# Optimization experiments

Measured on AMD Instinct MI355X. Metric: run time of the kernel, lower is better.

## Reference

```python
import jax, jax.numpy as jnp
import numpy as np

H = 128      # hidden_dim
N = 200000   # number of available (job, machine) ops
M = 1000     # machine nodes
J = 5000     # job nodes


def setup_inputs() -> dict:
    key = jax.random.key(0)
    ks = jax.random.split(key, 8)
    s = 0.05  # weight scale
    return {
        "x_graph": jax.random.normal(ks[0], (1, 2 * H), jnp.float32),
        "x_m": jax.random.normal(ks[1], (M, H), jnp.float32),
        "x_job": jax.random.normal(ks[2], (J, H), jnp.float32),
        "m_ids": jax.random.randint(ks[3], (N,), 0, M),
        "job_idx": jax.random.randint(ks[4], (N,), 0, J),
        "W0": jax.random.normal(ks[5], (4 * H, H), jnp.float32) * s,
        "b0": jnp.zeros((H,), jnp.float32),
        "W1": jax.random.normal(ks[6], (H, H), jnp.float32) * s,
        "b1": jnp.zeros((H,), jnp.float32),
        "W2": jax.random.normal(ks[7], (H, 1), jnp.float32) * s,
        "b2": jnp.zeros((1,), jnp.float32),
    }


def reference(x_graph, x_m, x_job, m_ids, job_idx, W0, b0, W1, b1, W2, b2):
    n = m_ids.shape[0]
    # vectorized form of the python loop: [x_graph | x_m[m_id] | x_job[job_pos]] -> [N, 4H]
    feats = jnp.concatenate(
        [
            jnp.broadcast_to(x_graph, (n, x_graph.shape[1])),
            x_m[m_ids],
            x_job[job_idx],
        ],
        axis=1,
    )
    h = jax.nn.relu(feats @ W0 + b0)   # Linear(4H -> H) + ReLU
    h = jax.nn.relu(h @ W1 + b1)       # Linear(H -> H) + ReLU
    scores = (h @ W2 + b2)[:, 0]       # Linear(H -> 1), squeeze -> [N]
    logp = jax.nn.log_softmax(scores, axis=0)
    probs = jnp.exp(logp)
    idx = jnp.argmax(scores)           # greedy selection (deterministic baseline)
    entropy = -jnp.sum(probs * logp)   # Categorical entropy
    return idx, probs[idx], logp[idx], entropy
```

## Files before the change

kernel.cpp:

```cpp
#include <hip/hip_runtime.h>
#include <math.h>

#define HID 128
#define TILE_R 64
#define TILE_P 32
#define XS_STRIDE 132
#define H0S_STRIDE 136
#define DELTA 0.05f
#define MAIN_GRID 1024

typedef short bf16x8 __attribute__((ext_vector_type(8)));
typedef float f32x4 __attribute__((ext_vector_type(4)));

static __device__ __forceinline__ unsigned short f2bf(float f) {
    union { float f; unsigned u; } v; v.f = f;
    unsigned r = v.u + 0x7FFFu + ((v.u >> 16) & 1u);
    return (unsigned short)(r >> 16);
}
static __device__ __forceinline__ float bflo(unsigned u) {
    union { unsigned u; float f; } v; v.u = u << 16; return v.f;
}
static __device__ __forceinline__ float bfhi(unsigned u) {
    union { unsigned u; float f; } v; v.u = u & 0xFFFF0000u; return v.f;
}

#define FMA4(avc, wv)                         \
    acc[r][0] = fmaf(avc, wv.x, acc[r][0]);   \
    acc[r][1] = fmaf(avc, wv.y, acc[r][1]);   \
    acc[r][2] = fmaf(avc, wv.z, acc[r][2]);   \
    acc[r][3] = fmaf(avc, wv.w, acc[r][3]);

__global__ __launch_bounds__(256, 4) void precompute_kernel(
    const float* __restrict__ x_graph,
    const float* __restrict__ x_m,
    const float* __restrict__ x_job,
    const float* __restrict__ W0,
    const float* __restrict__ b0,
    const float* __restrict__ W1,
    float* __restrict__ g,
    unsigned short* __restrict__ Pbf,
    unsigned short* __restrict__ W1T,
    int M, int J, int aTiles, int bTiles)
{
    const int t = threadIdx.x;
    const int bid = blockIdx.x;

    if (bid == 0) {
        __shared__ float xg[2 * HID];
        if (t < HID) { xg[t] = x_graph[t]; xg[t + HID] = x_graph[t + HID]; }
        __syncthreads();
        if (t < HID) {
            float acc = b0[t];
            #pragma unroll 8
            for (int k = 0; k < 2 * HID; ++k)
                acc = fmaf(xg[k], W0[k * HID + t], acc);
            g[t] = acc;
        }
        return;
    }
    if (bid == 1 + aTiles + bTiles) {
        for (int e = t; e < HID * HID; e += 256) {
            int n = e >> 7, k = e & 127;
            W1T[e] = f2bf(W1[k * HID + n]);
        }
        return;
    }

    const int tb = bid - 1;
    const float* X;
    const float* W;
    int r0, nr, dstBase;
    if (tb < aTiles) {
        r0 = tb * TILE_P;
        nr = min(TILE_P, M - r0);
        X = x_m + (size_t)r0 * HID;
        W = W0 + 2 * HID * HID;
        dstBase = r0;
    } else {
        int jb = tb - aTiles;
        r0 = jb * TILE_P;
        nr = min(TILE_P, J - r0);
        X = x_job + (size_t)r0 * HID;
        W = W0 + 3 * HID * HID;
        dstBase = M + r0;
    }

    __shared__ float xs[TILE_P * XS_STRIDE];
    {
        int row = t >> 3;
        int e = t & 7;
        #pragma unroll
        for (int u = 0; u < 4; ++u) {
            int c = e * 16 + u * 4;
            float4 v = (row < nr) ? *(const float4*)(X + row * HID + c)
                                  : make_float4(0.f, 0.f, 0.f, 0.f);
            *(float4*)&xs[row * XS_STRIDE + c] = v;
        }
    }
    __syncthreads();

    const int w = t >> 6;
    const int l = t & 63;
    const int tc = l & 7;
    const int tr = l >> 3;
    const int c0 = w * 32 + tc * 4;

    float acc[4][4];
    #pragma unroll
    for (int r = 0; r < 4; ++r)
        #pragma unroll
        for (int c = 0; c < 4; ++c) acc[r][c] = 0.0f;

    #pragma unroll 2
    for (int k0 = 0; k0 < HID; k0 += 4) {
        float4 w0v = *(const float4*)(W + (k0 + 0) * HID + c0);
        float4 w1v = *(const float4*)(W + (k0 + 1) * HID + c0);
        float4 w2m = *(const float4*)(W + (k0 + 2) * HID + c0);
        float4 w3v = *(const float4*)(W + (k0 + 3) * HID + c0);
        #pragma unroll
        for (int r = 0; r < 4; ++r) {
            float4 a = *(const float4*)&xs[(r * 8 + tr) * XS_STRIDE + k0];
            FMA4(a.x, w0v)
            FMA4(a.y, w1v)
            FMA4(a.z, w2m)
            FMA4(a.w, w3v)
        }
    }

    #pragma unroll
    for (int r = 0; r < 4; ++r) {
        int row = r * 8 + tr;
        if (row < nr) {
            unsigned lo0 = (unsigned)f2bf(acc[r][0]) | ((unsigned)f2bf(acc[r][1]) << 16);
            unsigned lo1 = (unsigned)f2bf(acc[r][2]) | ((unsigned)f2bf(acc[r][3]) << 16);
            uint2 pk = make_uint2(lo0, lo1);
            *(uint2*)(Pbf + (size_t)(dstBase + row) * HID + c0) = pk;
        }
    }
}

__global__ __launch_bounds__(256, 4) void main_kernel(
    const int* __restrict__ m_ids,
    const int* __restrict__ job_idx,
    const float* __restrict__ b1,
    const float* __restrict__ W2,
    const float* __restrict__ b2,
    const float* __restrict__ g,
    const unsigned short* __restrict__ Pbf,
    const unsigned short* __restrict__ W1T,
    float* __restrict__ scores,
    float4* __restrict__ partials,
    float* __restrict__ tmax,
    int N, int M, int tiles)
{
    __shared__ __align__(16) short h0s[TILE_R * H0S_STRIDE];
    __shared__ float sred[4 * TILE_R];

    const int t = threadIdx.x;
    const int l = t & 63;
    const int w = t >> 6;
    const int quad = l >> 4;
    const int mrow = l & 15;

    bf16x8 bfr[2][4];
    {
        const unsigned short* wb = W1T + (size_t)(w * 32 + mrow) * HID + quad * 8;
        #pragma unroll
        for (int nt = 0; nt < 2; ++nt)
            #pragma unroll
            for (int kc = 0; kc < 4; ++kc)
                bfr[nt][kc] = *(const bf16x8*)(wb + nt * 16 * HID + kc * 32);
    }
    const float b1v0 = b1[w * 32 + mrow];
    const float b1v1 = b1[w * 32 + 16 + mrow];
    const float w2v0 = W2[w * 32 + mrow];
    const float w2v1 = W2[w * 32 + 16 + mrow];
    const float b2v = b2[0];

    for (int tile = blockIdx.x; tile < tiles; tile += MAIN_GRID) {
        const int row0 = tile * TILE_R;

        {
            int row = t >> 2;
            int q = t & 3;
            int grow = row0 + row;
            int gr = (grow < N) ? grow : (N - 1);
            int m = m_ids[gr];
            int j = job_idx[gr];
            const unsigned short* pm = Pbf + (size_t)m * HID + q * 32;
            const unsigned short* pj = Pbf + (size_t)(M + j) * HID + q * 32;
            const float* gp = g + q * 32;
            short* dst = &h0s[row * H0S_STRIDE + q * 32];
            #pragma unroll
            for (int u = 0; u < 4; ++u) {
                uint4 mv = *(const uint4*)(pm + u * 8);
                uint4 jv = *(const uint4*)(pj + u * 8);
                float4 g0 = *(const float4*)(gp + u * 8);
                float4 g1 = *(const float4*)(gp + u * 8 + 4);
                float h0v = fmaxf(bflo(mv.x) + bflo(jv.x) + g0.x, 0.f);
                float h1v = fmaxf(bfhi(mv.x) + bfhi(jv.x) + g0.y, 0.f);
                float h2v = fmaxf(bflo(mv.y) + bflo(jv.y) + g0.z, 0.f);
                float h3v = fmaxf(bfhi(mv.y) + bfhi(jv.y) + g0.w, 0.f);
                float h4v = fmaxf(bflo(mv.z) + bflo(jv.z) + g1.x, 0.f);
                float h5v = fmaxf(bfhi(mv.z) + bfhi(jv.z) + g1.y, 0.f);
                float h6v = fmaxf(bflo(mv.w) + bflo(jv.w) + g1.z, 0.f);
                float h7v = fmaxf(bfhi(mv.w) + bfhi(jv.w) + g1.w, 0.f);
                uint4 pk;
                pk.x = (unsigned)f2bf(h0v) | ((unsigned)f2bf(h1v) << 16);
                pk.y = (unsigned)f2bf(h2v) | ((unsigned)f2bf(h3v) << 16);
                pk.z = (unsigned)f2bf(h4v) | ((unsigned)f2bf(h5v) << 16);
                pk.w = (unsigned)f2bf(h6v) | ((unsigned)f2bf(h7v) << 16);
                *(uint4*)(dst + u * 8) = pk;
            }
        }
        __syncthreads();

        f32x4 acc[4][2];
        #pragma unroll
        for (int mt = 0; mt < 4; ++mt) {
            f32x4 z = {0.f, 0.f, 0.f, 0.f};
            acc[mt][0] = z;
            acc[mt][1] = z;
        }
        #pragma unroll
        for (int mt = 0; mt < 4; ++mt) {
            const short* ab = &h0s[(mt * 16 + mrow) * H0S_STRIDE + quad * 8];
            #pragma unroll
            for (int kc = 0; kc < 4; ++kc) {
                bf16x8 af = *(const bf16x8*)(ab + kc * 32);
                acc[mt][0] = __builtin_amdgcn_mfma_f32_16x16x32_bf16(af, bfr[0][kc], acc[mt][0], 0, 0, 0);
                acc[mt][1] = __builtin_amdgcn_mfma_f32_16x16x32_bf16(af, bfr[1][kc], acc[mt][1], 0, 0, 0);
            }
        }

        #pragma unroll
        for (int mt = 0; mt < 4; ++mt) {
            float p[4];
            #pragma unroll
            for (int i = 0; i < 4; ++i) {
                p[i] = fmaxf(acc[mt][0][i] + b1v0, 0.f) * w2v0
                     + fmaxf(acc[mt][1][i] + b1v1, 0.f) * w2v1;
            }
            #pragma unroll
            for (int off = 1; off < 16; off <<= 1) {
                #pragma unroll
                for (int i = 0; i < 4; ++i)
                    p[i] += __shfl_xor(p[i], off);
            }
            if (mrow == 0) {
                int rb = mt * 16 + quad * 4;
                sred[w * TILE_R + rb + 0] = p[0];
                sred[w * TILE_R + rb + 1] = p[1];
                sred[w * TILE_R + rb + 2] = p[2];
                sred[w * TILE_R + rb + 3] = p[3];
            }
        }
        __syncthreads();

        if (t < 64) {
            int grow = row0 + t;
            float s = sred[t] + sred[64 + t] + sred[128 + t] + sred[192 + t] + b2v;
            if (grow < N) scores[grow] = s;
            else s = -1e30f;

            float mmax = s;
            int midx = grow;
            #pragma unroll
            for (int off = 1; off < 64; off <<= 1) {
                float om = __shfl_xor(mmax, off);
                int oi = __shfl_xor(midx, off);
                if (om > mmax || (om == mmax && oi < midx)) { mmax = om; midx = oi; }
            }
            float d = s - mmax;
            float e = expf(d);
            float z = e;
            float ss = d * e;
            #pragma unroll
            for (int off = 1; off < 64; off <<= 1) {
                z += __shfl_xor(z, off);
                ss += __shfl_xor(ss, off);
            }
            if (t == 0) {
                partials[tile] = make_float4(mmax, z, ss, (float)midx);
                tmax[tile] = mmax;
            }
        }
    }
}

__device__ inline void sm_merge(float& am, float& az, float& ass, int& ai,
                                float bm, float bz, float bss, int bi)
{
    if (bm > am || (bm == am && bi < ai)) {
        float tm = am, tz = az, ts = ass; int ti = ai;
        am = bm; az = bz; ass = bss; ai = bi;
        bm = tm; bz = tz; bss = ts; bi = ti;
    }
    float f = expf(bm - am);
    az += bz * f;
    ass += (bss + (bm - am) * bz) * f;
}

__global__ __launch_bounds__(256) void scan_kernel(
    const float* __restrict__ tmax, int nparts,
    const float* __restrict__ scores,
    const int* __restrict__ m_ids,
    const int* __restrict__ job_idx,
    const float* __restrict__ x_m,
    const float* __restrict__ x_job,
    const float* __restrict__ W0,
    const float* __restrict__ W1,
    const float* __restrict__ b1,
    const float* __restrict__ W2,
    const float* __restrict__ b2,
    const float* __restrict__ g,
    float2* __restrict__ bests,
    int N)
{
    __shared__ int cand[256];
    __shared__ int ccount;
    __shared__ float rs[4];
    __shared__ int ri[4];
    __shared__ float mmx[4];

    const int t = threadIdx.x;
    const int w = t >> 6;
    const int l = t & 63;
    const int base = blockIdx.x * 256;

    float m0 = -1e30f, m1 = -1e30f, m2 = -1e30f, m3 = -1e30f;
    int i = t;
    for (; i + 768 < nparts; i += 1024) {
        m0 = fmaxf(m0, tmax[i]);
        m1 = fmaxf(m1, tmax[i + 256]);
        m2 = fmaxf(m2, tmax[i + 512]);
        m3 = fmaxf(m3, tmax[i + 768]);
    }
    for (; i < nparts; i += 256) m0 = fmaxf(m0, tmax[i]);
    float mhat = fmaxf(fmaxf(m0, m1), fmaxf(m2, m3));
    #pragma unroll
    for (int off = 1; off < 64; off <<= 1)
        mhat = fmaxf(mhat, __shfl_xor(mhat, off));
    if (l == 0) mmx[w] = mhat;
    if (t == 0) ccount = 0;
    __syncthreads();
    mhat = fmaxf(fmaxf(mmx[0], mmx[1]), fmaxf(mmx[2], mmx[3]));
    const float cut = mhat - DELTA;

    int idx = base + t;
    if (idx < N && scores[idx] >= cut) {
        int p = atomicAdd(&ccount, 1);
        cand[p] = idx;
    }
    __syncthreads();
    const int nc = ccount;
    if (nc == 0) {
        if (t == 0) bests[blockIdx.x] = make_float2(-1e30f, __int_as_float(0x7fffffff));
        return;
    }

    float bs = -1e30f;
    int bi = 0x7fffffff;
    for (int c = w; c < nc; c += 4) {
        int gr = cand[c];
        int mm = m_ids[gr];
        int jj = job_idx[gr];
        const float* xm = x_m + (size_t)mm * HID;
        const float* xj = x_job + (size_t)jj * HID;
        const float* wm = W0 + 2 * HID * HID;
        const float* wj = W0 + 3 * HID * HID;
        float a0 = g[l], a1 = g[l + 64];
        for (int k = 0; k < HID; ++k) {
            float xmk = xm[k];
            float xjk = xj[k];
            a0 = fmaf(xmk, wm[k * HID + l], a0);
            a1 = fmaf(xmk, wm[k * HID + l + 64], a1);
            a0 = fmaf(xjk, wj[k * HID + l], a0);
            a1 = fmaf(xjk, wj[k * HID + l + 64], a1);
        }
        a0 = fmaxf(a0, 0.f);
        a1 = fmaxf(a1, 0.f);
        float acc0 = 0.f, acc1 = 0.f;
        for (int k = 0; k < 64; ++k) {
            float h = __shfl(a0, k);
            acc0 = fmaf(h, W1[k * HID + l], acc0);
            acc1 = fmaf(h, W1[k * HID + l + 64], acc1);
        }
        for (int k = 0; k < 64; ++k) {
            float h = __shfl(a1, k);
            acc0 = fmaf(h, W1[(k + 64) * HID + l], acc0);
            acc1 = fmaf(h, W1[(k + 64) * HID + l + 64], acc1);
        }
        float p = fmaxf(acc0 + b1[l], 0.f) * W2[l]
                + fmaxf(acc1 + b1[l + 64], 0.f) * W2[l + 64];
        #pragma unroll
        for (int off = 1; off < 64; off <<= 1)
            p += __shfl_xor(p, off);
        float s = p + b2[0];
        if (s > bs || (s == bs && gr < bi)) { bs = s; bi = gr; }
    }
    if (l == 0) { rs[w] = bs; ri[w] = bi; }
    __syncthreads();
    if (t == 0) {
        float best = rs[0];
        int bwin = ri[0];
        for (int i2 = 1; i2 < 4; ++i2)
            if (rs[i2] > best || (rs[i2] == best && ri[i2] < bwin)) {
                best = rs[i2]; bwin = ri[i2];
            }
        bests[blockIdx.x] = make_float2(best, __int_as_float(bwin));
    }
}

__global__ __launch_bounds__(256) void finalize_kernel(
    const float4* __restrict__ partials, int nparts,
    const float2* __restrict__ bests, int nblocks,
    float* __restrict__ out)
{
    __shared__ float4 wred[4];
    __shared__ int widx[4];
    __shared__ float rs[4];
    __shared__ int ri[4];
    const int t = threadIdx.x;
    const int w = t >> 6;
    const int l = t & 63;

    float m = -1e30f, z = 0.f, ss = 0.f;
    int idx = 0x7fffffff;
    for (int i = t; i < nparts; i += 256) {
        float4 p = partials[i];
        sm_merge(m, z, ss, idx, p.x, p.y, p.z, (int)p.w);
    }
    #pragma unroll
    for (int off = 1; off < 64; off <<= 1) {
        float om = __shfl_xor(m, off);
        float oz = __shfl_xor(z, off);
        float os = __shfl_xor(ss, off);
        int oi = __shfl_xor(idx, off);
        sm_merge(m, z, ss, idx, om, oz, os, oi);
    }
    if (l == 0) { wred[w] = make_float4(m, z, ss, 0.f); widx[w] = idx; }

    float bs = -1e30f;
    int bi = 0x7fffffff;
    for (int i = t; i < nblocks; i += 256) {
        float2 b = bests[i];
        int gi = __float_as_int(b.y);
        if (b.x > bs || (b.x == bs && gi < bi)) { bs = b.x; bi = gi; }
    }
    #pragma unroll
    for (int off = 1; off < 64; off <<= 1) {
        float os = __shfl_xor(bs, off);
        int oi = __shfl_xor(bi, off);
        if (os > bs || (os == bs && oi < bi)) { bs = os; bi = oi; }
    }
    if (l == 0) { rs[w] = bs; ri[w] = bi; }
    __syncthreads();

    if (t == 0) {
        for (int i = 1; i < 4; ++i) {
            sm_merge(m, z, ss, idx, wred[i].x, wred[i].y, wred[i].z, widx[i]);
            if (rs[i] > bs || (rs[i] == bs && ri[i] < bi)) { bs = rs[i]; bi = ri[i]; }
        }
        float logZ = logf(z);
        out[0] = (float)bi;
        out[1] = expf(bs - m) / z;
        out[2] = (bs - m) - logZ;
        out[3] = logZ - ss / z;
    }
}

extern "C" void kernel_launch(void* const* d_in, const int* in_sizes, int n_in,
                              void* d_out, int out_size, void* d_ws, size_t ws_size,
                              hipStream_t stream)
{
    const float* x_graph = (const float*)d_in[0];
    const float* x_m     = (const float*)d_in[1];
    const float* x_job   = (const float*)d_in[2];
    const int*   m_ids   = (const int*)d_in[3];
    const int*   job_idx = (const int*)d_in[4];
    const float* W0      = (const float*)d_in[5];
    const float* b0      = (const float*)d_in[6];
    const float* W1      = (const float*)d_in[7];
    const float* b1      = (const float*)d_in[8];
    const float* W2      = (const float*)d_in[9];
    const float* b2      = (const float*)d_in[10];
    float* out = (float*)d_out;

    const int N = in_sizes[3];
    const int M = in_sizes[1] / HID;
    const int J = in_sizes[2] / HID;

    const int tiles = (N + TILE_R - 1) / TILE_R;
    const int aTiles = (M + TILE_P - 1) / TILE_P;
    const int bTiles = (J + TILE_P - 1) / TILE_P;
    const int sblocks = (N + 255) / 256;

    float* ws = (float*)d_ws;
    float* g = ws;
    float* scores = ws + HID;
    float4* partials = (float4*)(scores + N);
    float* tmax = (float*)(partials + tiles);
    const int tmaxPad = (tiles + 3) & ~3;
    float2* bests = (float2*)(tmax + tmaxPad);
    unsigned short* W1T = (unsigned short*)(bests + sblocks + (sblocks & 1));
    unsigned short* Pbf = W1T + HID * HID;

    precompute_kernel<<<1 + aTiles + bTiles + 1, 256, 0, stream>>>(
        x_graph, x_m, x_job, W0, b0, W1, g, Pbf, W1T, M, J, aTiles, bTiles);
    main_kernel<<<MAIN_GRID, 256, 0, stream>>>(
        m_ids, job_idx, b1, W2, b2, g, Pbf, W1T, scores, partials, tmax,
        N, M, tiles);
    scan_kernel<<<sblocks, 256, 0, stream>>>(
        tmax, tiles, scores, m_ids, job_idx, x_m, x_job, W0, W1, b1, W2, b2,
        g, bests, N);
    finalize_kernel<<<1, 256, 0, stream>>>(partials, tiles, bests, sblocks, out);
}
```

Measured before the change: 139.7 us.

## Fuse four kernels into one persistent kernel with software grid barriers

Merges the precompute, main MLP, candidate scan and finalize kernels into a single persistent kernel of 1024 blocks, separated by atomic-counter grid barriers whose counters are zeroed by a memset. The W1 transpose is also split across 8 blocks instead of one. The aim is to remove kernel launch gaps and tail effects between the stages. In exchange it adds barrier spin costs and a memset launch, and relies on all 1024 blocks being co-resident; otherwise the kernel deadlocks.

```diff
diff --git a/kernel.cpp b/kernel.cpp
--- a/kernel.cpp
+++ b/kernel.cpp
@@ -7,7 +7,7 @@
 #define XS_STRIDE 132
 #define H0S_STRIDE 136
 #define DELTA 0.05f
-#define MAIN_GRID 1024
+#define GRID 1024
 
 typedef short bf16x8 __attribute__((ext_vector_type(8)));
 typedef float f32x4 __attribute__((ext_vector_type(4)));
@@ -30,266 +30,20 @@
     acc[r][2] = fmaf(avc, wv.z, acc[r][2]);   \
     acc[r][3] = fmaf(avc, wv.w, acc[r][3]);
 
-__global__ __launch_bounds__(256, 4) void precompute_kernel(
-    const float* __restrict__ x_graph,
-    const float* __restrict__ x_m,
-    const float* __restrict__ x_job,
-    const float* __restrict__ W0,
-    const float* __restrict__ b0,
-    const float* __restrict__ W1,
-    float* __restrict__ g,
-    unsigned short* __restrict__ Pbf,
-    unsigned short* __restrict__ W1T,
-    int M, int J, int aTiles, int bTiles)
-{
-    const int t = threadIdx.x;
-    const int bid = blockIdx.x;
-
-    if (bid == 0) {
-        __shared__ float xg[2 * HID];
-        if (t < HID) { xg[t] = x_graph[t]; xg[t + HID] = x_graph[t + HID]; }
-        __syncthreads();
-        if (t < HID) {
-            float acc = b0[t];
-            #pragma unroll 8
-            for (int k = 0; k < 2 * HID; ++k)
-                acc = fmaf(xg[k], W0[k * HID + t], acc);
-            g[t] = acc;
-        }
-        return;
-    }
-    if (bid == 1 + aTiles + bTiles) {
-        for (int e = t; e < HID * HID; e += 256) {
-            int n = e >> 7, k = e & 127;
-            W1T[e] = f2bf(W1[k * HID + n]);
-        }
-        return;
-    }
-
-    const int tb = bid - 1;
-    const float* X;
-    const float* W;
-    int r0, nr, dstBase;
-    if (tb < aTiles) {
-        r0 = tb * TILE_P;
-        nr = min(TILE_P, M - r0);
-        X = x_m + (size_t)r0 * HID;
-        W = W0 + 2 * HID * HID;
-        dstBase = r0;
-    } else {
-        int jb = tb - aTiles;
-        r0 = jb * TILE_P;
-        nr = min(TILE_P, J - r0);
-        X = x_job + (size_t)r0 * HID;
-        W = W0 + 3 * HID * HID;
-        dstBase = M + r0;
-    }
-
-    __shared__ float xs[TILE_P * XS_STRIDE];
-    {
-        int row = t >> 3;
-        int e = t & 7;
-        #pragma unroll
-        for (int u = 0; u < 4; ++u) {
-            int c = e * 16 + u * 4;
-            float4 v = (row < nr) ? *(const float4*)(X + row * HID + c)
-                                  : make_float4(0.f, 0.f, 0.f, 0.f);
-            *(float4*)&xs[row * XS_STRIDE + c] = v;
-        }
+static __device__ __forceinline__ void grid_barrier(int* counter) {
+    __syncthreads();
+    if (threadIdx.x == 0) {
+        __threadfence();
+        __hip_atomic_fetch_add(counter, 1, __ATOMIC_RELEASE, __HIP_MEMORY_SCOPE_AGENT);
+        while (__hip_atomic_load(counter, __ATOMIC_RELAXED, __HIP_MEMORY_SCOPE_AGENT) < GRID)
+            __builtin_amdgcn_s_sleep(1);
+        __threadfence();
     }
     __syncthreads();
-
-    const int w = t >> 6;
-    const int l = t & 63;
-    const int tc = l & 7;
-    const int tr = l >> 3;
-    const int c0 = w * 32 + tc * 4;
-
-    float acc[4][4];
-    #pragma unroll
-    for (int r = 0; r < 4; ++r)
-        #pragma unroll
-        for (int c = 0; c < 4; ++c) acc[r][c] = 0.0f;
-
-    #pragma unroll 2
-    for (int k0 = 0; k0 < HID; k0 += 4) {
-        float4 w0v = *(const float4*)(W + (k0 + 0) * HID + c0);
-        float4 w1v = *(const float4*)(W + (k0 + 1) * HID + c0);
-        float4 w2m = *(const float4*)(W + (k0 + 2) * HID + c0);
-        float4 w3v = *(const float4*)(W + (k0 + 3) * HID + c0);
-        #pragma unroll
-        for (int r = 0; r < 4; ++r) {
-            float4 a = *(const float4*)&xs[(r * 8 + tr) * XS_STRIDE + k0];
-            FMA4(a.x, w0v)
-            FMA4(a.y, w1v)
-            FMA4(a.z, w2m)
-            FMA4(a.w, w3v)
-        }
-    }
-
-    #pragma unroll
-    for (int r = 0; r < 4; ++r) {
-        int row = r * 8 + tr;
-        if (row < nr) {
-            unsigned lo0 = (unsigned)f2bf(acc[r][0]) | ((unsigned)f2bf(acc[r][1]) << 16);
-            unsigned lo1 = (unsigned)f2bf(acc[r][2]) | ((unsigned)f2bf(acc[r][3]) << 16);
-            uint2 pk = make_uint2(lo0, lo1);
-            *(uint2*)(Pbf + (size_t)(dstBase + row) * HID + c0) = pk;
-        }
-    }
-}
-
-__global__ __launch_bounds__(256, 4) void main_kernel(
-    const int* __restrict__ m_ids,
-    const int* __restrict__ job_idx,
-    const float* __restrict__ b1,
-    const float* __restrict__ W2,
-    const float* __restrict__ b2,
-    const float* __restrict__ g,
-    const unsigned short* __restrict__ Pbf,
-    const unsigned short* __restrict__ W1T,
-    float* __restrict__ scores,
-    float4* __restrict__ partials,
-    float* __restrict__ tmax,
-    int N, int M, int tiles)
-{
-    __shared__ __align__(16) short h0s[TILE_R * H0S_STRIDE];
-    __shared__ float sred[4 * TILE_R];
-
-    const int t = threadIdx.x;
-    const int l = t & 63;
-    const int w = t >> 6;
-    const int quad = l >> 4;
-    const int mrow = l & 15;
-
-    bf16x8 bfr[2][4];
-    {
-        const unsigned short* wb = W1T + (size_t)(w * 32 + mrow) * HID + quad * 8;
-        #pragma unroll
-        for (int nt = 0; nt < 2; ++nt)
-            #pragma unroll
-            for (int kc = 0; kc < 4; ++kc)
-                bfr[nt][kc] = *(const bf16x8*)(wb + nt * 16 * HID + kc * 32);
-    }
-    const float b1v0 = b1[w * 32 + mrow];
-    const float b1v1 = b1[w * 32 + 16 + mrow];
-    const float w2v0 = W2[w * 32 + mrow];
-    const float w2v1 = W2[w * 32 + 16 + mrow];
-    const float b2v = b2[0];
-
-    for (int tile = blockIdx.x; tile < tiles; tile += MAIN_GRID) {
-        const int row0 = tile * TILE_R;
-
-        {
-            int row = t >> 2;
-            int q = t & 3;
-            int grow = row0 + row;
-            int gr = (grow < N) ? grow : (N - 1);
-            int m = m_ids[gr];
-            int j = job_idx[gr];
-            const unsigned short* pm = Pbf + (size_t)m * HID + q * 32;
-            const unsigned short* pj = Pbf + (size_t)(M + j) * HID + q * 32;
-            const float* gp = g + q * 32;
-            short* dst = &h0s[row * H0S_STRIDE + q * 32];
-            #pragma unroll
-            for (int u = 0; u < 4; ++u) {
-                uint4 mv = *(const uint4*)(pm + u * 8);
-                uint4 jv = *(const uint4*)(pj + u * 8);
-                float4 g0 = *(const float4*)(gp + u * 8);
-                float4 g1 = *(const float4*)(gp + u * 8 + 4);
-                float h0v = fmaxf(bflo(mv.x) + bflo(jv.x) + g0.x, 0.f);
-                float h1v = fmaxf(bfhi(mv.x) + bfhi(jv.x) + g0.y, 0.f);
-                float h2v = fmaxf(bflo(mv.y) + bflo(jv.y) + g0.z, 0.f);
-                float h3v = fmaxf(bfhi(mv.y) + bfhi(jv.y) + g0.w, 0.f);
-                float h4v = fmaxf(bflo(mv.z) + bflo(jv.z) + g1.x, 0.f);
-                float h5v = fmaxf(bfhi(mv.z) + bfhi(jv.z) + g1.y, 0.f);
-                float h6v = fmaxf(bflo(mv.w) + bflo(jv.w) + g1.z, 0.f);
-                float h7v = fmaxf(bfhi(mv.w) + bfhi(jv.w) + g1.w, 0.f);
-                uint4 pk;
-                pk.x = (unsigned)f2bf(h0v) | ((unsigned)f2bf(h1v) << 16);
-                pk.y = (unsigned)f2bf(h2v) | ((unsigned)f2bf(h3v) << 16);
-                pk.z = (unsigned)f2bf(h4v) | ((unsigned)f2bf(h5v) << 16);
-                pk.w = (unsigned)f2bf(h6v) | ((unsigned)f2bf(h7v) << 16);
-                *(uint4*)(dst + u * 8) = pk;
-            }
-        }
-        __syncthreads();
-
-        f32x4 acc[4][2];
-        #pragma unroll
-        for (int mt = 0; mt < 4; ++mt) {
-            f32x4 z = {0.f, 0.f, 0.f, 0.f};
-            acc[mt][0] = z;
-            acc[mt][1] = z;
-        }
-        #pragma unroll
-        for (int mt = 0; mt < 4; ++mt) {
-            const short* ab = &h0s[(mt * 16 + mrow) * H0S_STRIDE + quad * 8];
-            #pragma unroll
-            for (int kc = 0; kc < 4; ++kc) {
-                bf16x8 af = *(const bf16x8*)(ab + kc * 32);
-                acc[mt][0] = __builtin_amdgcn_mfma_f32_16x16x32_bf16(af, bfr[0][kc], acc[mt][0], 0, 0, 0);
-                acc[mt][1] = __builtin_amdgcn_mfma_f32_16x16x32_bf16(af, bfr[1][kc], acc[mt][1], 0, 0, 0);
-            }
-        }
-
-        #pragma unroll
-        for (int mt = 0; mt < 4; ++mt) {
-            float p[4];
-            #pragma unroll
-            for (int i = 0; i < 4; ++i) {
-                p[i] = fmaxf(acc[mt][0][i] + b1v0, 0.f) * w2v0
-                     + fmaxf(acc[mt][1][i] + b1v1, 0.f) * w2v1;
-            }
-            #pragma unroll
-            for (int off = 1; off < 16; off <<= 1) {
-                #pragma unroll
-                for (int i = 0; i < 4; ++i)
-                    p[i] += __shfl_xor(p[i], off);
-            }
-            if (mrow == 0) {
-                int rb = mt * 16 + quad * 4;
-                sred[w * TILE_R + rb + 0] = p[0];
-                sred[w * TILE_R + rb + 1] = p[1];
-                sred[w * TILE_R + rb + 2] = p[2];
-                sred[w * TILE_R + rb + 3] = p[3];
-            }
-        }
-        __syncthreads();
-
-        if (t < 64) {
-            int grow = row0 + t;
-            float s = sred[t] + sred[64 + t] + sred[128 + t] + sred[192 + t] + b2v;
-            if (grow < N) scores[grow] = s;
-            else s = -1e30f;
-
-            float mmax = s;
-            int midx = grow;
-            #pragma unroll
-            for (int off = 1; off < 64; off <<= 1) {
-                float om = __shfl_xor(mmax, off);
-                int oi = __shfl_xor(midx, off);
-                if (om > mmax || (om == mmax && oi < midx)) { mmax = om; midx = oi; }
-            }
-            float d = s - mmax;
-            float e = expf(d);
-            float z = e;
-            float ss = d * e;
-            #pragma unroll
-            for (int off = 1; off < 64; off <<= 1) {
-                z += __shfl_xor(z, off);
-                ss += __shfl_xor(ss, off);
-            }
-            if (t == 0) {
-                partials[tile] = make_float4(mmax, z, ss, (float)midx);
-                tmax[tile] = mmax;
-            }
-        }
-    }
-}
-
-__device__ inline void sm_merge(float& am, float& az, float& ass, int& ai,
-                                float bm, float bz, float bss, int bi)
+}
+
+static __device__ __forceinline__ void sm_merge(float& am, float& az, float& ass, int& ai,
+                                                float bm, float bz, float bss, int bi)
 {
     if (bm > am || (bm == am && bi < ai)) {
         float tm = am, tz = az, ts = ass; int ti = ai;
@@ -301,172 +55,425 @@
     ass += (bss + (bm - am) * bz) * f;
 }
 
-__global__ __launch_bounds__(256) void scan_kernel(
-    const float* __restrict__ tmax, int nparts,
-    const float* __restrict__ scores,
+struct ScanSmem {
+    int cand[256];
+    int ccount;
+    float mmx[4];
+    float rs[4];
+    int ri[4];
+};
+struct FinSmem {
+    float4 wred[4];
+    int widx[4];
+    float rs[4];
+    int ri[4];
+};
+
+__global__ __launch_bounds__(256, 4) void fused_kernel(
+    const float* __restrict__ x_graph,
+    const float* __restrict__ x_m,
+    const float* __restrict__ x_job,
     const int* __restrict__ m_ids,
     const int* __restrict__ job_idx,
-    const float* __restrict__ x_m,
-    const float* __restrict__ x_job,
     const float* __restrict__ W0,
+    const float* __restrict__ b0,
     const float* __restrict__ W1,
     const float* __restrict__ b1,
     const float* __restrict__ W2,
     const float* __restrict__ b2,
-    const float* __restrict__ g,
+    int* __restrict__ bar,
+    float* __restrict__ g,
+    float* __restrict__ scores,
+    float4* __restrict__ partials,
+    float* __restrict__ tmax,
     float2* __restrict__ bests,
-    int N)
+    unsigned short* __restrict__ W1T,
+    unsigned short* __restrict__ Pbf,
+    float* __restrict__ out,
+    int N, int M, int J, int tiles, int aTiles, int bTiles, int sblocks)
 {
-    __shared__ int cand[256];
-    __shared__ int ccount;
-    __shared__ float rs[4];
-    __shared__ int ri[4];
-    __shared__ float mmx[4];
+    __shared__ __align__(16) unsigned char smem[TILE_R * H0S_STRIDE * 2 + TILE_R * 4 * 4];
 
     const int t = threadIdx.x;
-    const int w = t >> 6;
-    const int l = t & 63;
-    const int base = blockIdx.x * 256;
-
-    float m0 = -1e30f, m1 = -1e30f, m2 = -1e30f, m3 = -1e30f;
-    int i = t;
-    for (; i + 768 < nparts; i += 1024) {
-        m0 = fmaxf(m0, tmax[i]);
-        m1 = fmaxf(m1, tmax[i + 256]);
-        m2 = fmaxf(m2, tmax[i + 512]);
-        m3 = fmaxf(m3, tmax[i + 768]);
+    const int bid = blockIdx.x;
+
+    if (bid == 0) {
+        float* xg = (float*)smem;
+        if (t < HID) { xg[t] = x_graph[t]; xg[t + HID] = x_graph[t + HID]; }
+        __syncthreads();
+        if (t < HID) {
+            float acc = b0[t];
+            #pragma unroll 8
+            for (int k = 0; k < 2 * HID; ++k)
+                acc = fmaf(xg[k], W0[k * HID + t], acc);
+            g[t] = acc;
+        }
+    } else if (bid <= aTiles + bTiles) {
+        const int tb = bid - 1;
+        const float* X;
+        const float* W;
+        int r0, nr, dstBase;
+        if (tb < aTiles) {
+            r0 = tb * TILE_P;
+            nr = min(TILE_P, M - r0);
+            X = x_m + (size_t)r0 * HID;
+            W = W0 + 2 * HID * HID;
+            dstBase = r0;
+        } else {
+            int jb = tb - aTiles;
+            r0 = jb * TILE_P;
+            nr = min(TILE_P, J - r0);
+            X = x_job + (size_t)r0 * HID;
+            W = W0 + 3 * HID * HID;
+            dstBase = M + r0;
+        }
+
+        float* xs = (float*)smem;
+        {
+            int row = t >> 3;
+            int e = t & 7;
+            #pragma unroll
+            for (int u = 0; u < 4; ++u) {
+                int c = e * 16 + u * 4;
+                float4 v = (row < nr) ? *(const float4*)(X + row * HID + c)
+                                      : make_float4(0.f, 0.f, 0.f, 0.f);
+                *(float4*)&xs[row * XS_STRIDE + c] = v;
+            }
+        }
+        __syncthreads();
+
+        const int w = t >> 6;
+        const int l = t & 63;
+        const int tc = l & 7;
+        const int tr = l >> 3;
+        const int c0 = w * 32 + tc * 4;
+
+        float acc[4][4];
+        #pragma unroll
+        for (int r = 0; r < 4; ++r)
+            #pragma unroll
+            for (int c = 0; c < 4; ++c) acc[r][c] = 0.0f;
+
+        #pragma unroll 2
+        for (int k0 = 0; k0 < HID; k0 += 4) {
+            float4 w0v = *(const float4*)(W + (k0 + 0) * HID + c0);
+            float4 w1v = *(const float4*)(W + (k0 + 1) * HID + c0);
+            float4 w2m = *(const float4*)(W + (k0 + 2) * HID + c0);
+            float4 w3v = *(const float4*)(W + (k0 + 3) * HID + c0);
+            #pragma unroll
+            for (int r = 0; r < 4; ++r) {
+                float4 a = *(const float4*)&xs[(r * 8 + tr) * XS_STRIDE + k0];
+                FMA4(a.x, w0v)
+                FMA4(a.y, w1v)
+                FMA4(a.z, w2m)
+                FMA4(a.w, w3v)
+            }
+        }
+
+        #pragma unroll
+        for (int r = 0; r < 4; ++r) {
+            int row = r * 8 + tr;
+            if (row < nr) {
+                unsigned lo0 = (unsigned)f2bf(acc[r][0]) | ((unsigned)f2bf(acc[r][1]) << 16);
+                unsigned lo1 = (unsigned)f2bf(acc[r][2]) | ((unsigned)f2bf(acc[r][3]) << 16);
+                uint2 pk = make_uint2(lo0, lo1);
+                *(uint2*)(Pbf + (size_t)(dstBase + row) * HID + c0) = pk;
+            }
+        }
+    } else if (bid <= aTiles + bTiles + 8) {
+        int part = bid - (aTiles + bTiles + 1);
+        int e0 = part * (HID * HID / 8);
+        for (int e = e0 + t; e < e0 + HID * HID / 8; e += 256) {
+            int n = e >> 7, k = e & 127;
+            W1T[e] = f2bf(W1[k * HID + n]);
+        }
     }
-    for (; i < nparts; i += 256) m0 = fmaxf(m0, tmax[i]);
-    float mhat = fmaxf(fmaxf(m0, m1), fmaxf(m2, m3));
-    #pragma unroll
-    for (int off = 1; off < 64; off <<= 1)
-        mhat = fmaxf(mhat, __shfl_xor(mhat, off));
-    if (l == 0) mmx[w] = mhat;
-    if (t == 0) ccount = 0;
-    __syncthreads();
-    mhat = fmaxf(fmaxf(mmx[0], mmx[1]), fmaxf(mmx[2], mmx[3]));
-    const float cut = mhat - DELTA;
-
-    int idx = base + t;
-    if (idx < N && scores[idx] >= cut) {
-        int p = atomicAdd(&ccount, 1);
-        cand[p] = idx;
+
+    grid_barrier(&bar[0]);
+
+    {
+        short* h0s = (short*)smem;
+        float* sred = (float*)(smem + TILE_R * H0S_STRIDE * 2);
+
+        const int l = t & 63;
+        const int w = t >> 6;
+        const int quad = l >> 4;
+        const int mrow = l & 15;
+
+        bf16x8 bfr[2][4];
+        {
+            const unsigned short* wb = W1T + (size_t)(w * 32 + mrow) * HID + quad * 8;
+            #pragma unroll
+            for (int nt = 0; nt < 2; ++nt)
+                #pragma unroll
+                for (int kc = 0; kc < 4; ++kc)
+                    bfr[nt][kc] = *(const bf16x8*)(wb + nt * 16 * HID + kc * 32);
+        }
+        const float b1v0 = b1[w * 32 + mrow];
+        const float b1v1 = b1[w * 32 + 16 + mrow];
+        const float w2v0 = W2[w * 32 + mrow];
+        const float w2v1 = W2[w * 32 + 16 + mrow];
+        const float b2v = b2[0];
+
+        for (int tile = bid; tile < tiles; tile += GRID) {
+            const int row0 = tile * TILE_R;
+
+            {
+                int row = t >> 2;
+                int q = t & 3;
+                int grow = row0 + row;
+                int gr = (grow < N) ? grow : (N - 1);
+                int m = m_ids[gr];
+                int j = job_idx[gr];
+                const unsigned short* pm = Pbf + (size_t)m * HID + q * 32;
+                const unsigned short* pj = Pbf + (size_t)(M + j) * HID + q * 32;
+                const float* gp = g + q * 32;
+                short* dst = &h0s[row * H0S_STRIDE + q * 32];
+                #pragma unroll
+                for (int u = 0; u < 4; ++u) {
+                    uint4 mv = *(const uint4*)(pm + u * 8);
+                    uint4 jv = *(const uint4*)(pj + u * 8);
+                    float4 g0 = *(const float4*)(gp + u * 8);
+                    float4 g1 = *(const float4*)(gp + u * 8 + 4);
+                    float h0v = fmaxf(bflo(mv.x) + bflo(jv.x) + g0.x, 0.f);
+                    float h1v = fmaxf(bfhi(mv.x) + bfhi(jv.x) + g0.y, 0.f);
+                    float h2v = fmaxf(bflo(mv.y) + bflo(jv.y) + g0.z, 0.f);
+                    float h3v = fmaxf(bfhi(mv.y) + bfhi(jv.y) + g0.w, 0.f);
+                    float h4v = fmaxf(bflo(mv.z) + bflo(jv.z) + g1.x, 0.f);
+                    float h5v = fmaxf(bfhi(mv.z) + bfhi(jv.z) + g1.y, 0.f);
+                    float h6v = fmaxf(bflo(mv.w) + bflo(jv.w) + g1.z, 0.f);
+                    float h7v = fmaxf(bfhi(mv.w) + bfhi(jv.w) + g1.w, 0.f);
+                    uint4 pk;
+                    pk.x = (unsigned)f2bf(h0v) | ((unsigned)f2bf(h1v) << 16);
+                    pk.y = (unsigned)f2bf(h2v) | ((unsigned)f2bf(h3v) << 16);
+                    pk.z = (unsigned)f2bf(h4v) | ((unsigned)f2bf(h5v) << 16);
+                    pk.w = (unsigned)f2bf(h6v) | ((unsigned)f2bf(h7v) << 16);
+                    *(uint4*)(dst + u * 8) = pk;
+                }
+            }
+            __syncthreads();
+
+            f32x4 acc[4][2];
+            #pragma unroll
+            for (int mt = 0; mt < 4; ++mt) {
+                f32x4 z = {0.f, 0.f, 0.f, 0.f};
+                acc[mt][0] = z;
+                acc[mt][1] = z;
+            }
+            #pragma unroll
+            for (int mt = 0; mt < 4; ++mt) {
+                const short* ab = &h0s[(mt * 16 + mrow) * H0S_STRIDE + quad * 8];
+                #pragma unroll
+                for (int kc = 0; kc < 4; ++kc) {
+                    bf16x8 af = *(const bf16x8*)(ab + kc * 32);
+                    acc[mt][0] = __builtin_amdgcn_mfma_f32_16x16x32_bf16(af, bfr[0][kc], acc[mt][0], 0, 0, 0);
+                    acc[mt][1] = __builtin_amdgcn_mfma_f32_16x16x32_bf16(af, bfr[1][kc], acc[mt][1], 0, 0, 0);
+                }
+            }
+
+            #pragma unroll
+            for (int mt = 0; mt < 4; ++mt) {
+                float p[4];
+                #pragma unroll
+                for (int i = 0; i < 4; ++i) {
+                    p[i] = fmaxf(acc[mt][0][i] + b1v0, 0.f) * w2v0
+                         + fmaxf(acc[mt][1][i] + b1v1, 0.f) * w2v1;
+                }
+                #pragma unroll
+                for (int off = 1; off < 16; off <<= 1) {
+                    #pragma unroll
+                    for (int i = 0; i < 4; ++i)
+                        p[i] += __shfl_xor(p[i], off);
+                }
+                if (mrow == 0) {
+                    int rb = mt * 16 + quad * 4;
+                    sred[w * TILE_R + rb + 0] = p[0];
+                    sred[w * TILE_R + rb + 1] = p[1];
+                    sred[w * TILE_R + rb + 2] = p[2];
+                    sred[w * TILE_R + rb + 3] = p[3];
+                }
+            }
+            __syncthreads();
+
+            if (t < 64) {
+                int grow = row0 + t;
+                float s = sred[t] + sred[64 + t] + sred[128 + t] + sred[192 + t] + b2v;
+                if (grow < N) scores[grow] = s;
+                else s = -1e30f;
+
+                float mmax = s;
+                int midx = grow;
+                #pragma unroll
+                for (int off = 1; off < 64; off <<= 1) {
+                    float om = __shfl_xor(mmax, off);
+                    int oi = __shfl_xor(midx, off);
+                    if (om > mmax || (om == mmax && oi < midx)) { mmax = om; midx = oi; }
+                }
+                float d = s - mmax;
+                float e = expf(d);
+                float z = e;
+                float ss = d * e;
+                #pragma unroll
+                for (int off = 1; off < 64; off <<= 1) {
+                    z += __shfl_xor(z, off);
+                    ss += __shfl_xor(ss, off);
+                }
+                if (t == 0) {
+                    partials[tile] = make_float4(mmax, z, ss, (float)midx);
+                    tmax[tile] = mmax;
+                }
+            }
+        }
     }
-    __syncthreads();
-    const int nc = ccount;
-    if (nc == 0) {
-        if (t == 0) bests[blockIdx.x] = make_float2(-1e30f, __int_as_float(0x7fffffff));
-        return;
-    }
-
-    float bs = -1e30f;
-    int bi = 0x7fffffff;
-    for (int c = w; c < nc; c += 4) {
-        int gr = cand[c];
-        int mm = m_ids[gr];
-        int jj = job_idx[gr];
-        const float* xm = x_m + (size_t)mm * HID;
-        const float* xj = x_job + (size_t)jj * HID;
-        const float* wm = W0 + 2 * HID * HID;
-        const float* wj = W0 + 3 * HID * HID;
-        float a0 = g[l], a1 = g[l + 64];
-        for (int k = 0; k < HID; ++k) {
-            float xmk = xm[k];
-            float xjk = xj[k];
-            a0 = fmaf(xmk, wm[k * HID + l], a0);
-            a1 = fmaf(xmk, wm[k * HID + l + 64], a1);
-            a0 = fmaf(xjk, wj[k * HID + l], a0);
-            a1 = fmaf(xjk, wj[k * HID + l + 64], a1);
-        }
-        a0 = fmaxf(a0, 0.f);
-        a1 = fmaxf(a1, 0.f);
-        float acc0 = 0.f, acc1 = 0.f;
-        for (int k = 0; k < 64; ++k) {
-            float h = __shfl(a0, k);
-            acc0 = fmaf(h, W1[k * HID + l], acc0);
-            acc1 = fmaf(h, W1[k * HID + l + 64], acc1);
-        }
-        for (int k = 0; k < 64; ++k) {
-            float h = __shfl(a1, k);
-            acc0 = fmaf(h, W1[(k + 64) * HID + l], acc0);
-            acc1 = fmaf(h, W1[(k + 64) * HID + l + 64], acc1);
-        }
-        float p = fmaxf(acc0 + b1[l], 0.f) * W2[l]
-                + fmaxf(acc1 + b1[l + 64], 0.f) * W2[l + 64];
+
+    grid_barrier(&bar[32]);
+
+    {
+        ScanSmem* ss = (ScanSmem*)smem;
+        const int w = t >> 6;
+        const int l = t & 63;
+
+        float m0 = -1e30f, m1 = -1e30f, m2 = -1e30f, m3 = -1e30f;
+        int i = t;
+        for (; i + 768 < tiles; i += 1024) {
+            m0 = fmaxf(m0, tmax[i]);
+            m1 = fmaxf(m1, tmax[i + 256]);
+            m2 = fmaxf(m2, tmax[i + 512]);
+            m3 = fmaxf(m3, tmax[i + 768]);
+        }
+        for (; i < tiles; i += 256) m0 = fmaxf(m0, tmax[i]);
+        float mhat = fmaxf(fmaxf(m0, m1), fmaxf(m2, m3));
         #pragma unroll
         for (int off = 1; off < 64; off <<= 1)
-            p += __shfl_xor(p, off);
-        float s = p + b2[0];
-        if (s > bs || (s == bs && gr < bi)) { bs = s; bi = gr; }
+            mhat = fmaxf(mhat, __shfl_xor(mhat, off));
+        if (l == 0) ss->mmx[w] = mhat;
+        __syncthreads();
+        mhat = fmaxf(fmaxf(ss->mmx[0], ss->mmx[1]), fmaxf(ss->mmx[2], ss->mmx[3]));
+        const float cut = mhat - DELTA;
+
+        for (int chunk = bid; chunk < sblocks; chunk += GRID) {
+            const int base = chunk * 256;
+            if (t == 0) ss->ccount = 0;
+            __syncthreads();
+
+            int idx = base + t;
+            if (idx < N && scores[idx] >= cut) {
+                int p = atomicAdd(&ss->ccount, 1);
+                ss->cand[p] = idx;
+            }
+            __syncthreads();
+            const int nc = ss->ccount;
+
+            if (nc == 0) {
+                if (t == 0) bests[chunk] = make_float2(-1e30f, __int_as_float(0x7fffffff));
+            } else {
+                float bs = -1e30f;
+                int bi = 0x7fffffff;
+                for (int c = w; c < nc; c += 4) {
+                    int gr = ss->cand[c];
+                    int mm = m_ids[gr];
+                    int jj = job_idx[gr];
+                    const float* xm = x_m + (size_t)mm * HID;
+                    const float* xj = x_job + (size_t)jj * HID;
+                    const float* wm = W0 + 2 * HID * HID;
+                    const float* wj = W0 + 3 * HID * HID;
+                    float a0 = g[l], a1 = g[l + 64];
+                    for (int k = 0; k < HID; ++k) {
+                        float xmk = xm[k];
+                        float xjk = xj[k];
+                        a0 = fmaf(xmk, wm[k * HID + l], a0);
+                        a1 = fmaf(xmk, wm[k * HID + l + 64], a1);
+                        a0 = fmaf(xjk, wj[k * HID + l], a0);
+                        a1 = fmaf(xjk, wj[k * HID + l + 64], a1);
+                    }
+                    a0 = fmaxf(a0, 0.f);
+                    a1 = fmaxf(a1, 0.f);
+                    float acc0 = 0.f, acc1 = 0.f;
+                    for (int k = 0; k < 64; ++k) {
+                        float h = __shfl(a0, k);
+                        acc0 = fmaf(h, W1[k * HID + l], acc0);
+                        acc1 = fmaf(h, W1[k * HID + l + 64], acc1);
+                    }
+                    for (int k = 0; k < 64; ++k) {
+                        float h = __shfl(a1, k);
+                        acc0 = fmaf(h, W1[(k + 64) * HID + l], acc0);
+                        acc1 = fmaf(h, W1[(k + 64) * HID + l + 64], acc1);
+                    }
+                    float p = fmaxf(acc0 + b1[l], 0.f) * W2[l]
+                            + fmaxf(acc1 + b1[l + 64], 0.f) * W2[l + 64];
+                    #pragma unroll
+                    for (int off = 1; off < 64; off <<= 1)
+                        p += __shfl_xor(p, off);
+                    float s = p + b2[0];
+                    if (s > bs || (s == bs && gr < bi)) { bs = s; bi = gr; }
+                }
+                if (l == 0) { ss->rs[w] = bs; ss->ri[w] = bi; }
+                __syncthreads();
+                if (t == 0) {
+                    float best = ss->rs[0];
+                    int bwin = ss->ri[0];
+                    for (int i2 = 1; i2 < 4; ++i2)
+                        if (ss->rs[i2] > best || (ss->rs[i2] == best && ss->ri[i2] < bwin)) {
+                            best = ss->rs[i2]; bwin = ss->ri[i2];
+                        }
+                    bests[chunk] = make_float2(best, __int_as_float(bwin));
+                }
+            }
+            __syncthreads();
+        }
     }
-    if (l == 0) { rs[w] = bs; ri[w] = bi; }
-    __syncthreads();
-    if (t == 0) {
-        float best = rs[0];
-        int bwin = ri[0];
-        for (int i2 = 1; i2 < 4; ++i2)
-            if (rs[i2] > best || (rs[i2] == best && ri[i2] < bwin)) {
-                best = rs[i2]; bwin = ri[i2];
-            }
-        bests[blockIdx.x] = make_float2(best, __int_as_float(bwin));
-    }
-}
-
-__global__ __launch_bounds__(256) void finalize_kernel(
-    const float4* __restrict__ partials, int nparts,
-    const float2* __restrict__ bests, int nblocks,
-    float* __restrict__ out)
-{
-    __shared__ float4 wred[4];
-    __shared__ int widx[4];
-    __shared__ float rs[4];
-    __shared__ int ri[4];
-    const int t = threadIdx.x;
-    const int w = t >> 6;
-    const int l = t & 63;
-
-    float m = -1e30f, z = 0.f, ss = 0.f;
-    int idx = 0x7fffffff;
-    for (int i = t; i < nparts; i += 256) {
-        float4 p = partials[i];
-        sm_merge(m, z, ss, idx, p.x, p.y, p.z, (int)p.w);
-    }
-    #pragma unroll
-    for (int off = 1; off < 64; off <<= 1) {
-        float om = __shfl_xor(m, off);
-        float oz = __shfl_xor(z, off);
-        float os = __shfl_xor(ss, off);
-        int oi = __shfl_xor(idx, off);
-        sm_merge(m, z, ss, idx, om, oz, os, oi);
-    }
-    if (l == 0) { wred[w] = make_float4(m, z, ss, 0.f); widx[w] = idx; }
-
-    float bs = -1e30f;
-    int bi = 0x7fffffff;
-    for (int i = t; i < nblocks; i += 256) {
-        float2 b = bests[i];
-        int gi = __float_as_int(b.y);
-        if (b.x > bs || (b.x == bs && gi < bi)) { bs = b.x; bi = gi; }
-    }
-    #pragma unroll
-    for (int off = 1; off < 64; off <<= 1) {
-        float os = __shfl_xor(bs, off);
-        int oi = __shfl_xor(bi, off);
-        if (os > bs || (os == bs && oi < bi)) { bs = os; bi = oi; }
-    }
-    if (l == 0) { rs[w] = bs; ri[w] = bi; }
-    __syncthreads();
-
-    if (t == 0) {
-        for (int i = 1; i < 4; ++i) {
-            sm_merge(m, z, ss, idx, wred[i].x, wred[i].y, wred[i].z, widx[i]);
-            if (rs[i] > bs || (rs[i] == bs && ri[i] < bi)) { bs = rs[i]; bi = ri[i]; }
-        }
-        float logZ = logf(z);
-        out[0] = (float)bi;
-        out[1] = expf(bs - m) / z;
-        out[2] = (bs - m) - logZ;
-        out[3] = logZ - ss / z;
+
+    grid_barrier(&bar[64]);
+
+    if (bid != 0) return;
+    {
+        FinSmem* fs = (FinSmem*)smem;
+        const int w = t >> 6;
+        const int l = t & 63;
+
+        float m = -1e30f, z = 0.f, ssum = 0.f;
+        int idx = 0x7fffffff;
+        for (int i = t; i < tiles; i += 256) {
+            float4 p = partials[i];
+            sm_merge(m, z, ssum, idx, p.x, p.y, p.z, (int)p.w);
+        }
+        #pragma unroll
+        for (int off = 1; off < 64; off <<= 1) {
+            float om = __shfl_xor(m, off);
+            float oz = __shfl_xor(z, off);
+            float os = __shfl_xor(ssum, off);
+            int oi = __shfl_xor(idx, off);
+            sm_merge(m, z, ssum, idx, om, oz, os, oi);
+        }
+        if (l == 0) { fs->wred[w] = make_float4(m, z, ssum, 0.f); fs->widx[w] = idx; }
+
+        float bs = -1e30f;
+        int bi = 0x7fffffff;
+        for (int i = t; i < sblocks; i += 256) {
+            float2 b = bests[i];
+            int gi = __float_as_int(b.y);
+            if (b.x > bs || (b.x == bs && gi < bi)) { bs = b.x; bi = gi; }
+        }
+        #pragma unroll
+        for (int off = 1; off < 64; off <<= 1) {
+            float os = __shfl_xor(bs, off);
+            int oi = __shfl_xor(bi, off);
+            if (os > bs || (os == bs && oi < bi)) { bs = os; bi = oi; }
+        }
+        if (l == 0) { fs->rs[w] = bs; fs->ri[w] = bi; }
+        __syncthreads();
+
+        if (t == 0) {
+            for (int i = 1; i < 4; ++i) {
+                sm_merge(m, z, ssum, idx, fs->wred[i].x, fs->wred[i].y, fs->wred[i].z, fs->widx[i]);
+                if (fs->rs[i] > bs || (fs->rs[i] == bs && fs->ri[i] < bi)) { bs = fs->rs[i]; bi = fs->ri[i]; }
+            }
+            float logZ = logf(z);
+            out[0] = (float)bi;
+            out[1] = expf(bs - m) / z;
+            out[2] = (bs - m) - logZ;
+            out[3] = logZ - ssum / z;
+        }
     }
 }
 
@@ -496,7 +503,8 @@
     const int bTiles = (J + TILE_P - 1) / TILE_P;
     const int sblocks = (N + 255) / 256;
 
-    float* ws = (float*)d_ws;
+    int* bar = (int*)d_ws;
+    float* ws = (float*)d_ws + 128;
     float* g = ws;
     float* scores = ws + HID;
     float4* partials = (float4*)(scores + N);
@@ -506,13 +514,9 @@
     unsigned short* W1T = (unsigned short*)(bests + sblocks + (sblocks & 1));
     unsigned short* Pbf = W1T + HID * HID;
 
-    precompute_kernel<<<1 + aTiles + bTiles + 1, 256, 0, stream>>>(
-        x_graph, x_m, x_job, W0, b0, W1, g, Pbf, W1T, M, J, aTiles, bTiles);
-    main_kernel<<<MAIN_GRID, 256, 0, stream>>>(
-        m_ids, job_idx, b1, W2, b2, g, Pbf, W1T, scores, partials, tmax,
-        N, M, tiles);
-    scan_kernel<<<sblocks, 256, 0, stream>>>(
-        tmax, tiles, scores, m_ids, job_idx, x_m, x_job, W0, W1, b1, W2, b2,
-        g, bests, N);
-    finalize_kernel<<<1, 256, 0, stream>>>(partials, tiles, bests, sblocks, out);
-}
+    hipMemsetAsync(d_ws, 0, 512, stream);
+    fused_kernel<<<GRID, 256, 0, stream>>>(
+        x_graph, x_m, x_job, m_ids, job_idx, W0, b0, W1, b1, W2, b2,
+        bar, g, scores, partials, tmax, bests, W1T, Pbf, out,
+        N, M, J, tiles, aTiles, bTiles, sblocks);
+}
```

Result: slower. 436.2 us (+212.3%).
